# Performance work log

Hardware: AMD Instinct MI355X
Metric: run time of the kernel (lower is better)

Reference implementation:

```python
import jax, jax.numpy as jnp
import numpy as np

SCALING = 2.0  # lora alpha / rank
B, S, H = 4, 2048, 4096
N = 4096  # q/k/v out features
R = 16    # lora rank


def setup_inputs() -> dict:
    key = jax.random.key(0)
    ks = jax.random.split(key, 10)
    std_w = 1.0 / np.sqrt(H)
    inp = {
        'X': jax.random.normal(ks[0], (B, S, H), dtype=jnp.float32),
        'QW': jax.random.normal(ks[1], (N, H), dtype=jnp.float32) * std_w,
        'QA': jax.random.normal(ks[2], (R, H), dtype=jnp.float32) * std_w,
        'QB': jax.random.normal(ks[3], (N, R), dtype=jnp.float32) * 0.01,
        'KW': jax.random.normal(ks[4], (N, H), dtype=jnp.float32) * std_w,
        'KA': jax.random.normal(ks[5], (R, H), dtype=jnp.float32) * std_w,
        'KB': jax.random.normal(ks[6], (N, R), dtype=jnp.float32) * 0.01,
        'VW': jax.random.normal(ks[7], (N, H), dtype=jnp.float32) * std_w,
        'VA': jax.random.normal(ks[8], (R, H), dtype=jnp.float32) * std_w,
        'VB': jax.random.normal(ks[9], (N, R), dtype=jnp.float32) * 0.01,
    }
    return inp


def _matmul_lora(X, W, A, Bm, scaling):
    # Y = X @ W.T + scaling * (X @ A.T) @ B.T ; X: [bs, h], W: [n, h], A: [r, h], B: [n, r]
    base = jnp.einsum('bsh,nh->bsn', X, W)
    lora = jnp.einsum('bsr,nr->bsn', jnp.einsum('bsh,rh->bsr', X, A), Bm)
    return base + scaling * lora


def reference(X, QW, QA, QB, KW, KA, KB, VW, VA, VB):
    Q = _matmul_lora(X, QW, QA, QB, SCALING)
    K = _matmul_lora(X, KW, KA, KB, SCALING)
    V = _matmul_lora(X, VW, VA, VB, SCALING)
    return (Q, K, V)
```

## Files before the change

### kernel.cpp

```cpp
#include <hip/hip_runtime.h>


typedef unsigned short u16;
typedef __attribute__((ext_vector_type(4))) float  f32x4;
typedef __attribute__((ext_vector_type(8))) __bf16 bf16x8;
typedef __attribute__((ext_vector_type(8))) short  s16x8;

#define MDIM 8192
#define NDIM 4096
#define KDIM 4096

__device__ __forceinline__ u16 f2bf(float f) {
    union { float f; unsigned int u; } v;
    v.f = f;
    unsigned int r = v.u + 0x7FFFu + ((v.u >> 16) & 1u);
    return (u16)(r >> 16);
}

__global__ void __launch_bounds__(256) cvt_x_kernel(const float* __restrict__ X,
                                                    u16* __restrict__ Xb, int nvec8) {
    int stride = gridDim.x * blockDim.x;
    for (int i = blockIdx.x * blockDim.x + threadIdx.x; i < nvec8; i += stride) {
        f32x4 x0 = ((const f32x4*)X)[2 * i];
        f32x4 x1 = ((const f32x4*)X)[2 * i + 1];
        s16x8 o;
        o[0] = (short)f2bf(x0[0]); o[1] = (short)f2bf(x0[1]);
        o[2] = (short)f2bf(x0[2]); o[3] = (short)f2bf(x0[3]);
        o[4] = (short)f2bf(x1[0]); o[5] = (short)f2bf(x1[1]);
        o[6] = (short)f2bf(x1[2]); o[7] = (short)f2bf(x1[3]);
        ((s16x8*)Xb)[i] = o;
    }
}

__global__ void __launch_bounds__(256) merge_w_kernel(const float* __restrict__ W,
                                                      const float* __restrict__ A,
                                                      const float* __restrict__ Bm,
                                                      u16* __restrict__ Wb) {
    __shared__ float As[16][64];
    const int t  = threadIdx.x;
    const int hb = blockIdx.x * 64;
    const int nb = blockIdx.y * 128;

    {
        int r = t >> 4, c = (t & 15) * 4;
        *(f32x4*)&As[r][c] = *(const f32x4*)&A[r * 4096 + hb + c];
    }
    __syncthreads();

    const int hl = (t & 7) * 8;
    const int n0 = nb + (t >> 3) * 4;

    float bv[4][16];
    float s[4][8];
#pragma unroll
    for (int i = 0; i < 4; i++) {
        const float* br = &Bm[(size_t)(n0 + i) * 16];
#pragma unroll
        for (int r = 0; r < 16; r++) bv[i][r] = 2.0f * br[r];
        f32x4 w0 = *(const f32x4*)&W[(size_t)(n0 + i) * 4096 + hb + hl];
        f32x4 w1 = *(const f32x4*)&W[(size_t)(n0 + i) * 4096 + hb + hl + 4];
        s[i][0] = w0[0]; s[i][1] = w0[1]; s[i][2] = w0[2]; s[i][3] = w0[3];
        s[i][4] = w1[0]; s[i][5] = w1[1]; s[i][6] = w1[2]; s[i][7] = w1[3];
    }
#pragma unroll
    for (int r = 0; r < 16; r++) {
        f32x4 a0 = *(const f32x4*)&As[r][hl];
        f32x4 a1 = *(const f32x4*)&As[r][hl + 4];
#pragma unroll
        for (int i = 0; i < 4; i++) {
            s[i][0] += bv[i][r] * a0[0]; s[i][1] += bv[i][r] * a0[1];
            s[i][2] += bv[i][r] * a0[2]; s[i][3] += bv[i][r] * a0[3];
            s[i][4] += bv[i][r] * a1[0]; s[i][5] += bv[i][r] * a1[1];
            s[i][6] += bv[i][r] * a1[2]; s[i][7] += bv[i][r] * a1[3];
        }
    }
#pragma unroll
    for (int i = 0; i < 4; i++) {
        s16x8 o;
#pragma unroll
        for (int j = 0; j < 8; j++) o[j] = (short)f2bf(s[i][j]);
        *(s16x8*)&Wb[(size_t)(n0 + i) * 4096 + hb + hl] = o;
    }
}


#define BM 256
#define BN 256
#define BK 64
#define NKT (KDIM / BK)

#define BAR() __builtin_amdgcn_s_barrier()
#define WAIT_LGKM0() asm volatile("s_waitcnt lgkmcnt(0)" ::: "memory")
#define WAIT_VM(n) asm volatile("s_waitcnt vmcnt(" #n ")" ::: "memory")
#define PRIO(p) __builtin_amdgcn_s_setprio(p)

__global__ void __launch_bounds__(512, 2) gemm8_kernel(const u16* __restrict__ Xb,
                                                       const u16* __restrict__ Wb,
                                                       float* __restrict__ out) {
    extern __shared__ char lds[];

    const int t    = threadIdx.x;
    const int lane = t & 63;
    const int w    = t >> 6;
    const int wr   = w >> 2;
    const int wn   = w & 3;
    const int lr   = lane & 15;
    const int lkq  = lane >> 4;
    const int lr7  = lr & 7;

    int wg = blockIdx.x;
    wg = (wg & 7) * 192 + (wg >> 3);
    const int z  = wg >> 9;
    const int r_ = wg & 511;
    const int nT = r_ & 15;
    const int mT = r_ >> 4;
    const int mBase = mT * BM;
    const int nBase = nT * BN;

    const u16* Wp = Wb + (size_t)z * NDIM * KDIM;
    const char* gA = (const char*)Xb + (size_t)mBase * (KDIM * 2);
    const char* gB = (const char*)Wp + (size_t)nBase * (KDIM * 2);

    char* ldsA0 = lds;
    char* ldsA1 = lds + 32768;
    char* ldsB0 = lds + 65536;
    char* ldsB1 = lds + 98304;

    const int blkrow = lane >> 3;
    const int colswz = ((lane & 7) ^ blkrow) << 4;
    const size_t stg0 = (size_t)(((w << 1) | 0) * 8 + blkrow) * (KDIM * 2) + colswz;
    const size_t stg1 = (size_t)(((w << 1) | 1) * 8 + blkrow) * (KDIM * 2) + colswz;
    const int ldsStg0 = (((w << 1) | 0) << 10) + lane * 16;
    const int ldsStg1 = (((w << 1) | 1) << 10) + lane * 16;

#define STAGE(ldsTile, gtile, h, kt)                                              \
  { __builtin_amdgcn_global_load_lds(                                             \
        (const __attribute__((address_space(1))) void*)((gtile) + stg0 +          \
            (size_t)(h) * (128 * KDIM * 2) + (size_t)(kt) * 128),                 \
        (__attribute__((address_space(3))) void*)((ldsTile) + (h) * 16384 + ldsStg0), \
        16, 0, 0);                                                                \
    __builtin_amdgcn_global_load_lds(                                             \
        (const __attribute__((address_space(1))) void*)((gtile) + stg1 +          \
            (size_t)(h) * (128 * KDIM * 2) + (size_t)(kt) * 128),                 \
        (__attribute__((address_space(3))) void*)((ldsTile) + (h) * 16384 + ldsStg1), \
        16, 0, 0); }

    const int csA = (lkq << 4) ^ (lr7 << 4);
    const int rA0 = (wr * 128 + lr) * 128;
    const int rB0 = (wn * 64 + lr) * 128;
#define RD_A(tile, mi, kk) (*(const bf16x8*)((tile) + rA0 + (mi) * 2048 + (((kk) << 6) ^ csA)))
#define RD_B(tile, ni, kk) (*(const bf16x8*)((tile) + rB0 + (ni) * 2048 + (((kk) << 6) ^ csA)))

    f32x4 acc[8][4] = {};
    bf16x8 aR1[4][2], aR2[4][2], bR[4][2];

#define MFMA_Q(AF, mbase, nbase)                                                   \
    PRIO(1);                                                                       \
    _Pragma("unroll") for (int mi = 0; mi < 4; ++mi)                               \
    _Pragma("unroll") for (int ni = 0; ni < 2; ++ni)                               \
    _Pragma("unroll") for (int kk = 0; kk < 2; ++kk)                               \
      acc[(mbase) + mi][(nbase) + ni] = __builtin_amdgcn_mfma_f32_16x16x32_bf16(   \
          AF[mi][kk], bR[(nbase) + ni][kk], acc[(mbase) + mi][(nbase) + ni], 0, 0, 0); \
    PRIO(0);

#define PH1(pA, pB, STG)                                                           \
  { _Pragma("unroll") for (int mi = 0; mi < 4; ++mi) {                             \
      aR1[mi][0] = RD_A(pA, mi, 0); aR1[mi][1] = RD_A(pA, mi, 1); }                \
    _Pragma("unroll") for (int ni = 0; ni < 4; ++ni) {                             \
      bR[ni][0] = RD_B(pB, ni, 0); bR[ni][1] = RD_B(pB, ni, 1); }                  \
    STG; BAR(); WAIT_LGKM0(); MFMA_Q(aR1, 0, 0) BAR(); }

#define PH2(pA, STG)                                                               \
  { aR2[0][0] = RD_A(pA, 4, 0); aR2[0][1] = RD_A(pA, 4, 1);                        \
    aR2[1][0] = RD_A(pA, 5, 0); aR2[1][1] = RD_A(pA, 5, 1);                        \
    STG; BAR(); WAIT_LGKM0(); MFMA_Q(aR1, 0, 2) BAR(); }

#define PH3(pA, STG)                                                               \
  { aR2[2][0] = RD_A(pA, 6, 0); aR2[2][1] = RD_A(pA, 6, 1);                        \
    aR2[3][0] = RD_A(pA, 7, 0); aR2[3][1] = RD_A(pA, 7, 1);                        \
    STG; BAR(); WAIT_LGKM0(); MFMA_Q(aR2, 4, 0) BAR(); }

#define PH4(STG, VMW)                                                              \
  { STG; VMW; BAR(); WAIT_LGKM0(); MFMA_Q(aR2, 4, 2) BAR(); }

    STAGE(ldsA0, gA, 0, 0); STAGE(ldsA0, gA, 1, 0);
    STAGE(ldsB0, gB, 0, 0); STAGE(ldsB0, gB, 1, 0);
    STAGE(ldsB1, gB, 0, 1); STAGE(ldsB1, gB, 1, 1);
    STAGE(ldsA1, gA, 0, 1);
    WAIT_VM(6);
    BAR();

    for (int i = 0; i < 31; ++i) {
        const int tt = 2 * i;
        PH1(ldsA0, ldsB0, STAGE(ldsA1, gA, 1, tt + 1));
        PH2(ldsA0,        STAGE(ldsB0, gB, 0, tt + 2));
        PH3(ldsA0,        STAGE(ldsB0, gB, 1, tt + 2));
        PH4(              STAGE(ldsA0, gA, 0, tt + 2), WAIT_VM(6));
        PH1(ldsA1, ldsB1, STAGE(ldsA0, gA, 1, tt + 2));
        PH2(ldsA1,        STAGE(ldsB1, gB, 0, tt + 3));
        PH3(ldsA1,        STAGE(ldsB1, gB, 1, tt + 3));
        PH4(              STAGE(ldsA1, gA, 0, tt + 3), WAIT_VM(6));
    }

    PH1(ldsA0, ldsB0, STAGE(ldsA1, gA, 1, 63));
    PH2(ldsA0, );
    PH3(ldsA0, );
    PH4(, WAIT_VM(0));
    PH1(ldsA1, ldsB1, );
    PH2(ldsA1, );
    PH3(ldsA1, );
    PH4(, );

    float* C = out + (size_t)z * MDIM * NDIM;
#pragma unroll
    for (int mi = 0; mi < 8; ++mi) {
#pragma unroll
        for (int ni = 0; ni < 4; ++ni) {
            const int col  = nBase + wn * 64 + ni * 16 + lr;
            const int row0 = mBase + wr * 128 + mi * 16 + lkq * 4;
            f32x4 v = acc[mi][ni];
#pragma unroll
            for (int j = 0; j < 4; ++j)
                C[(size_t)(row0 + j) * NDIM + col] = v[j];
        }
    }
}

extern "C" void kernel_launch(void* const* d_in, const int* in_sizes, int n_in,
                              void* d_out, int out_size, void* d_ws, size_t ws_size,
                              hipStream_t stream) {
    const float* X  = (const float*)d_in[0];
    const float* QW = (const float*)d_in[1];
    const float* QA = (const float*)d_in[2];
    const float* QB = (const float*)d_in[3];
    const float* KW = (const float*)d_in[4];
    const float* KA = (const float*)d_in[5];
    const float* KB = (const float*)d_in[6];
    const float* VW = (const float*)d_in[7];
    const float* VA = (const float*)d_in[8];
    const float* VB = (const float*)d_in[9];
    float* out = (float*)d_out;

    u16* Xb = (u16*)d_ws;
    u16* Wb = (u16*)((char*)d_ws + (size_t)MDIM * KDIM * 2);

    static bool attr_done = false;
    if (!attr_done) {
        (void)hipFuncSetAttribute((const void*)gemm8_kernel,
                                  hipFuncAttributeMaxDynamicSharedMemorySize, 131072);
        attr_done = true;
    }

    cvt_x_kernel<<<2048, 256, 0, stream>>>(X, Xb, (MDIM * KDIM) / 8);

    dim3 wgrid(4096 / 64, 4096 / 128);
    merge_w_kernel<<<wgrid, 256, 0, stream>>>(QW, QA, QB, Wb + (size_t)0 * NDIM * KDIM);
    merge_w_kernel<<<wgrid, 256, 0, stream>>>(KW, KA, KB, Wb + (size_t)1 * NDIM * KDIM);
    merge_w_kernel<<<wgrid, 256, 0, stream>>>(VW, VA, VB, Wb + (size_t)2 * NDIM * KDIM);

    gemm8_kernel<<<dim3(16 * 32 * 3), dim3(512), 131072, stream>>>(Xb, Wb, out);
}
```

Measured before the change: 802.1 us.

## Rebalance GEMM LDS read/stage schedule, fuse merge kernels, use nontemporal stores

Moves half of the B-fragment LDS reads from phase 1 into phase 2 and reorders the global-to-LDS staging across phases, with adjusted vmcnt waits and one LDS wait dropped in phase 4. The aim is to spread LDS and global traffic more evenly between MFMA bursts. It also merges the three LoRA weight-merge launches into a single 3D-grid launch and writes the fp32 output with nontemporal stores so it bypasses caching. The reshuffled waits carry a risk of LDS read/write hazards if the new ordering is not exactly right.

```diff
diff --git a/kernel.cpp b/kernel.cpp
--- a/kernel.cpp
+++ b/kernel.cpp
@@ -32,10 +32,22 @@
     }
 }
 
-__global__ void __launch_bounds__(256) merge_w_kernel(const float* __restrict__ W,
-                                                      const float* __restrict__ A,
-                                                      const float* __restrict__ Bm,
-                                                      u16* __restrict__ Wb) {
+__global__ void __launch_bounds__(256) merge_w3_kernel(const float* __restrict__ QW,
+                                                       const float* __restrict__ QA,
+                                                       const float* __restrict__ QB,
+                                                       const float* __restrict__ KW,
+                                                       const float* __restrict__ KA,
+                                                       const float* __restrict__ KB,
+                                                       const float* __restrict__ VW,
+                                                       const float* __restrict__ VA,
+                                                       const float* __restrict__ VB,
+                                                       u16* __restrict__ WbAll) {
+    const int z = blockIdx.z;
+    const float* W  = (z == 0) ? QW : (z == 1) ? KW : VW;
+    const float* A  = (z == 0) ? QA : (z == 1) ? KA : VA;
+    const float* Bm = (z == 0) ? QB : (z == 1) ? KB : VB;
+    u16* Wb = WbAll + (size_t)z * NDIM * KDIM;
+
     __shared__ float As[16][64];
     const int t  = threadIdx.x;
     const int hb = blockIdx.x * 64;
@@ -87,10 +99,10 @@
 #define BM 256
 #define BN 256
 #define BK 64
-#define NKT (KDIM / BK)
 
 #define BAR() __builtin_amdgcn_s_barrier()
 #define WAIT_LGKM0() asm volatile("s_waitcnt lgkmcnt(0)" ::: "memory")
+#define LGKM_HINT8() asm volatile("s_waitcnt lgkmcnt(8)" ::: "memory")
 #define WAIT_VM(n) asm volatile("s_waitcnt vmcnt(" #n ")" ::: "memory")
 #define PRIO(p) __builtin_amdgcn_s_setprio(p)
 
@@ -166,12 +178,14 @@
 #define PH1(pA, pB, STG)                                                           \
   { _Pragma("unroll") for (int mi = 0; mi < 4; ++mi) {                             \
       aR1[mi][0] = RD_A(pA, mi, 0); aR1[mi][1] = RD_A(pA, mi, 1); }                \
-    _Pragma("unroll") for (int ni = 0; ni < 4; ++ni) {                             \
-      bR[ni][0] = RD_B(pB, ni, 0); bR[ni][1] = RD_B(pB, ni, 1); }                  \
-    STG; BAR(); WAIT_LGKM0(); MFMA_Q(aR1, 0, 0) BAR(); }
-
-#define PH2(pA, STG)                                                               \
-  { aR2[0][0] = RD_A(pA, 4, 0); aR2[0][1] = RD_A(pA, 4, 1);                        \
+    bR[0][0] = RD_B(pB, 0, 0); bR[0][1] = RD_B(pB, 0, 1);                          \
+    bR[1][0] = RD_B(pB, 1, 0); bR[1][1] = RD_B(pB, 1, 1);                          \
+    STG; LGKM_HINT8(); BAR(); WAIT_LGKM0(); MFMA_Q(aR1, 0, 0) BAR(); }
+
+#define PH2(pA, pB, STG)                                                           \
+  { bR[2][0] = RD_B(pB, 2, 0); bR[2][1] = RD_B(pB, 2, 1);                          \
+    bR[3][0] = RD_B(pB, 3, 0); bR[3][1] = RD_B(pB, 3, 1);                          \
+    aR2[0][0] = RD_A(pA, 4, 0); aR2[0][1] = RD_A(pA, 4, 1);                        \
     aR2[1][0] = RD_A(pA, 5, 0); aR2[1][1] = RD_A(pA, 5, 1);                        \
     STG; BAR(); WAIT_LGKM0(); MFMA_Q(aR1, 0, 2) BAR(); }
 
@@ -181,7 +195,10 @@
     STG; BAR(); WAIT_LGKM0(); MFMA_Q(aR2, 4, 0) BAR(); }
 
 #define PH4(STG, VMW)                                                              \
-  { STG; VMW; BAR(); WAIT_LGKM0(); MFMA_Q(aR2, 4, 2) BAR(); }
+  { STG; VMW; BAR(); MFMA_Q(aR2, 4, 2) BAR(); }
+
+#define PH4F()                                                                     \
+  { BAR(); MFMA_Q(aR2, 4, 2) }
 
     STAGE(ldsA0, gA, 0, 0); STAGE(ldsA0, gA, 1, 0);
     STAGE(ldsB0, gB, 0, 0); STAGE(ldsB0, gB, 1, 0);
@@ -191,25 +208,26 @@
     BAR();
 
     for (int i = 0; i < 31; ++i) {
-        const int tt = 2 * i;
-        PH1(ldsA0, ldsB0, STAGE(ldsA1, gA, 1, tt + 1));
-        PH2(ldsA0,        STAGE(ldsB0, gB, 0, tt + 2));
-        PH3(ldsA0,        STAGE(ldsB0, gB, 1, tt + 2));
-        PH4(              STAGE(ldsA0, gA, 0, tt + 2), WAIT_VM(6));
-        PH1(ldsA1, ldsB1, STAGE(ldsA0, gA, 1, tt + 2));
-        PH2(ldsA1,        STAGE(ldsB1, gB, 0, tt + 3));
-        PH3(ldsA1,        STAGE(ldsB1, gB, 1, tt + 3));
-        PH4(              STAGE(ldsA1, gA, 0, tt + 3), WAIT_VM(6));
+        const int T = 2 * i;
+        PH1(ldsA0, ldsB0, STAGE(ldsA1, gA, 1, T + 1));
+        PH2(ldsA0, ldsB0, );
+        PH3(ldsA0,        STAGE(ldsB0, gB, 0, T + 2));
+        PH4(              STAGE(ldsB0, gB, 1, T + 2), WAIT_VM(4));
+        PH1(ldsA1, ldsB1, STAGE(ldsA0, gA, 0, T + 2));
+        PH2(ldsA1, ldsB1, STAGE(ldsA0, gA, 1, T + 2));
+        PH3(ldsA1,        STAGE(ldsB1, gB, 0, T + 3));
+        PH4(              { STAGE(ldsB1, gB, 1, T + 3)
+                            STAGE(ldsA1, gA, 0, T + 3) }, WAIT_VM(6));
     }
 
     PH1(ldsA0, ldsB0, STAGE(ldsA1, gA, 1, 63));
-    PH2(ldsA0, );
+    PH2(ldsA0, ldsB0, );
     PH3(ldsA0, );
     PH4(, WAIT_VM(0));
     PH1(ldsA1, ldsB1, );
-    PH2(ldsA1, );
+    PH2(ldsA1, ldsB1, );
     PH3(ldsA1, );
-    PH4(, );
+    PH4F();
 
     float* C = out + (size_t)z * MDIM * NDIM;
 #pragma unroll
@@ -221,7 +239,7 @@
             f32x4 v = acc[mi][ni];
 #pragma unroll
             for (int j = 0; j < 4; ++j)
-                C[(size_t)(row0 + j) * NDIM + col] = v[j];
+                __builtin_nontemporal_store(v[j], &C[(size_t)(row0 + j) * NDIM + col]);
         }
     }
 }
@@ -244,19 +262,13 @@
     u16* Xb = (u16*)d_ws;
     u16* Wb = (u16*)((char*)d_ws + (size_t)MDIM * KDIM * 2);
 
-    static bool attr_done = false;
-    if (!attr_done) {
-        (void)hipFuncSetAttribute((const void*)gemm8_kernel,
-                                  hipFuncAttributeMaxDynamicSharedMemorySize, 131072);
-        attr_done = true;
-    }
+    (void)hipFuncSetAttribute((const void*)gemm8_kernel,
+                              hipFuncAttributeMaxDynamicSharedMemorySize, 131072);
 
     cvt_x_kernel<<<2048, 256, 0, stream>>>(X, Xb, (MDIM * KDIM) / 8);
 
-    dim3 wgrid(4096 / 64, 4096 / 128);
-    merge_w_kernel<<<wgrid, 256, 0, stream>>>(QW, QA, QB, Wb + (size_t)0 * NDIM * KDIM);
-    merge_w_kernel<<<wgrid, 256, 0, stream>>>(KW, KA, KB, Wb + (size_t)1 * NDIM * KDIM);
-    merge_w_kernel<<<wgrid, 256, 0, stream>>>(VW, VA, VB, Wb + (size_t)2 * NDIM * KDIM);
+    dim3 wgrid(4096 / 64, 4096 / 128, 3);
+    merge_w3_kernel<<<wgrid, 256, 0, stream>>>(QW, QA, QB, KW, KA, KB, VW, VA, VB, Wb);
 
     gemm8_kernel<<<dim3(16 * 32 * 3), dim3(512), 131072, stream>>>(Xb, Wb, out);
 }
```

Result: no change. 807.0 us (+0.6%).
